# Kernel optimization log

Measured on AMD Instinct MI355X. Metric: run time of the kernel, lower is better.

The kernel has to match this reference:

```python
import jax, jax.numpy as jnp
import numpy as np


def setup_inputs() -> dict:
    key = jax.random.key(0)
    kA, kB = jax.random.split(key)
    B, H, W, C = 8, 48, 48, 256
    feature_A = jax.random.normal(kA, (B, H, W, C), dtype=jnp.float32)
    feature_B = jax.random.normal(kB, (B, H, W, C), dtype=jnp.float32)
    return {"feature_A": feature_A, "feature_B": feature_B}


def reference(feature_A, feature_B):
    # corr[b,i,j,k,l] = mean_c A[b,i,j,c] * B[b,k,l,c]
    # Expressed as a batched GEMM over the channel dim instead of the
    # naive [B,H,W,H,W,C] broadcast intermediate.
    C = feature_A.shape[-1]
    corr = jnp.einsum('bijc,bklc->bijkl', feature_A, feature_B) / C
    # L2 norm over source positions (i,j) per target position (k,l)
    penalty = jnp.sqrt(jnp.sum(corr * corr, axis=(1, 2), keepdims=True))  # [B,1,1,H,W]
    return corr / penalty
```

## Files before the change

kernel.cpp:

```cpp
#include <hip/hip_runtime.h>


#define HW2 2304
#define CH  256
#define NB  8
#define NELEM (NB * HW2 * CH)
#define KS  6

typedef __attribute__((ext_vector_type(8))) short bf16x8;
typedef __attribute__((ext_vector_type(4))) float f32x4;

static __device__ inline unsigned short f2bf(float f) {
    union { float f; unsigned u; } x; x.f = f;
    unsigned r = x.u + 0x7FFFu + ((x.u >> 16) & 1u);
    return (unsigned short)(r >> 16);
}

static __device__ inline float bf2f(unsigned short u) {
    union { unsigned u; float f; } x; x.u = ((unsigned)u) << 16;
    return x.f;
}

static __device__ inline void async_copy16(const void* g, void* l) {
    __builtin_amdgcn_global_load_lds(
        (const __attribute__((address_space(1))) unsigned int*)g,
        (__attribute__((address_space(3))) unsigned int*)l, 16, 0, 0);
}

__global__ __launch_bounds__(256) void convert_bf16(const float* __restrict__ A,
                                                    const float* __restrict__ B,
                                                    unsigned short* __restrict__ Abf,
                                                    unsigned short* __restrict__ Bbf,
                                                    unsigned short* __restrict__ Atbf) {
    __shared__ unsigned short t[64][65];
    const int blk = blockIdx.x;
    const bool isA = blk < 1152;
    const int tb = isA ? blk : blk - 1152;
    const int b  = tb / 144;
    const int tt = tb % 144;
    const int ijt = tt >> 2, ct = tt & 3;
    const size_t base = ((size_t)b * HW2 + (size_t)ijt * 64) * CH + ct * 64;
    const float* src = (isA ? A : B) + base;
    unsigned short* dst = (isA ? Abf : Bbf) + base;
    const int tid = threadIdx.x;
    const int lr = tid & 15, rq = tid >> 4;
#pragma unroll
    for (int p = 0; p < 4; p++) {
        const int row = rq + p * 16;
        float4 v = *(const float4*)(src + (size_t)row * CH + lr * 4);
        ushort4 u;
        u.x = f2bf(v.x); u.y = f2bf(v.y); u.z = f2bf(v.z); u.w = f2bf(v.w);
        *(ushort4*)(dst + (size_t)row * CH + lr * 4) = u;
        if (isA) {
            t[row][lr * 4 + 0] = u.x; t[row][lr * 4 + 1] = u.y;
            t[row][lr * 4 + 2] = u.z; t[row][lr * 4 + 3] = u.w;
        }
    }
    if (isA) {
        __syncthreads();
#pragma unroll
        for (int p = 0; p < 4; p++) {
            const int c = rq + p * 16;
            ushort4 u;
            u.x = t[lr * 4 + 0][c]; u.y = t[lr * 4 + 1][c];
            u.z = t[lr * 4 + 2][c]; u.w = t[lr * 4 + 3][c];
            *(ushort4*)(Atbf + ((size_t)b * CH + (size_t)(ct * 64 + c)) * HW2
                        + (size_t)ijt * 64 + lr * 4) = u;
        }
    }
}

__global__ __launch_bounds__(256) void gram_partial(const unsigned short* __restrict__ Atbf,
                                                    float* __restrict__ Gf) {
    __shared__ unsigned short As[2 * 128 * 32];
    __shared__ unsigned short Bs[2 * 128 * 32];
    const int tid = threadIdx.x;
    const int bx = blockIdx.x, by = blockIdx.y;
    const int b  = blockIdx.z / KS, ks = blockIdx.z % KS;
    const int kt0 = ks * (HW2 / KS);

    const unsigned short* Ar = Atbf + ((size_t)b * CH + by * 128) * HW2;
    const unsigned short* Br = Atbf + ((size_t)b * CH + bx * 128) * HW2;

    const int srow = tid >> 2, skcol = (tid & 3) * 8;
    const int wave = tid >> 6, lane = tid & 63;
    const int wm = (wave >> 1) * 64, wn = (wave & 1) * 64;
    const int lr = lane & 15, quad = lane >> 4, k8 = quad * 8;

    f32x4 acc[4][4];
#pragma unroll
    for (int i = 0; i < 4; i++)
#pragma unroll
        for (int j = 0; j < 4; j++) acc[i][j] = (f32x4){0.f, 0.f, 0.f, 0.f};

    for (int kt = kt0; kt < kt0 + HW2 / KS; kt += 64) {
#pragma unroll
        for (int c = 0; c < 2; c++) {
            const int kof = kt + c * 32;
#pragma unroll
            for (int i = 0; i < 2; i++) {
                async_copy16(Ar + (size_t)(srow + i * 64) * HW2 + kof + skcol,
                             &As[c * 4096 + tid * 8 + i * 2048]);
                async_copy16(Br + (size_t)(srow + i * 64) * HW2 + kof + skcol,
                             &Bs[c * 4096 + tid * 8 + i * 2048]);
            }
        }
        __syncthreads();
#pragma unroll
        for (int c = 0; c < 2; c++) {
            bf16x8 af[4], bfr[4];
#pragma unroll
            for (int mt = 0; mt < 4; mt++)
                af[mt] = *(const bf16x8*)&As[c * 4096 + (wm + mt * 16 + lr) * 32 + k8];
#pragma unroll
            for (int nt = 0; nt < 4; nt++)
                bfr[nt] = *(const bf16x8*)&Bs[c * 4096 + (wn + nt * 16 + lr) * 32 + k8];
#pragma unroll
            for (int mt = 0; mt < 4; mt++)
#pragma unroll
                for (int nt = 0; nt < 4; nt++)
                    acc[mt][nt] = __builtin_amdgcn_mfma_f32_16x16x32_bf16(
                        af[mt], bfr[nt], acc[mt][nt], 0, 0, 0);
        }
        __syncthreads();
    }
#pragma unroll
    for (int mt = 0; mt < 4; mt++)
#pragma unroll
        for (int nt = 0; nt < 4; nt++) {
            f32x4 v = acc[mt][nt];
            const int row = by * 128 + wm + mt * 16 + quad * 4;
            const int col = bx * 128 + wn + nt * 16 + lr;
#pragma unroll
            for (int r = 0; r < 4; r++)
                atomicAdd(&Gf[((size_t)b * CH + row + r) * CH + col], v[r]);
        }
}

__global__ __launch_bounds__(256) void g_to_bf(const float* __restrict__ Gf,
                                               unsigned short* __restrict__ Gbf) {
    const int i = blockIdx.x * 256 + threadIdx.x;
    float4 v = ((const float4*)Gf)[i];
    ushort4 u;
    u.x = f2bf(v.x); u.y = f2bf(v.y); u.z = f2bf(v.z); u.w = f2bf(v.w);
    ((ushort4*)Gbf)[i] = u;
}

__global__ __launch_bounds__(256) void colsq_pass(const unsigned short* __restrict__ Bbf,
                                                  const unsigned short* __restrict__ Gbf,
                                                  float* __restrict__ colSqG) {
    __shared__ unsigned short As[2 * 128 * 32];
    __shared__ unsigned short Bs[2 * 128 * 32];
    const int tid = threadIdx.x;
    const int bx = blockIdx.x;
    const int by = blockIdx.y;
    const int b  = blockIdx.z;

    const unsigned short* Ab = Bbf + ((size_t)b * HW2 + by * 128) * CH;
    const unsigned short* Gb = Gbf + ((size_t)b * CH + bx * 128) * CH;

    const int srow = tid >> 2, skcol = (tid & 3) * 8;
    const int wave = tid >> 6, lane = tid & 63;
    const int wm = (wave >> 1) * 64, wn = (wave & 1) * 64;
    const int lr = lane & 15, quad = lane >> 4, k8 = quad * 8;

    f32x4 acc[4][4];
#pragma unroll
    for (int i = 0; i < 4; i++)
#pragma unroll
        for (int j = 0; j < 4; j++) acc[i][j] = (f32x4){0.f, 0.f, 0.f, 0.f};

    for (int kt = 0; kt < CH; kt += 64) {
#pragma unroll
        for (int c = 0; c < 2; c++) {
            const int kof = kt + c * 32;
#pragma unroll
            for (int i = 0; i < 2; i++) {
                async_copy16(Ab + (size_t)(srow + i * 64) * CH + kof + skcol,
                             &As[c * 4096 + tid * 8 + i * 2048]);
                async_copy16(Gb + (size_t)(srow + i * 64) * CH + kof + skcol,
                             &Bs[c * 4096 + tid * 8 + i * 2048]);
            }
        }
        __syncthreads();
#pragma unroll
        for (int c = 0; c < 2; c++) {
            bf16x8 af[4], bfr[4];
#pragma unroll
            for (int mt = 0; mt < 4; mt++)
                af[mt] = *(const bf16x8*)&As[c * 4096 + (wm + mt * 16 + lr) * 32 + k8];
#pragma unroll
            for (int nt = 0; nt < 4; nt++)
                bfr[nt] = *(const bf16x8*)&Bs[c * 4096 + (wn + nt * 16 + lr) * 32 + k8];
#pragma unroll
            for (int mt = 0; mt < 4; mt++)
#pragma unroll
                for (int nt = 0; nt < 4; nt++)
                    acc[mt][nt] = __builtin_amdgcn_mfma_f32_16x16x32_bf16(
                        af[mt], bfr[nt], acc[mt][nt], 0, 0, 0);
        }
        __syncthreads();
    }

    const unsigned short* Brow = Ab + bx * 128;
#pragma unroll
    for (int mt = 0; mt < 4; mt++)
#pragma unroll
        for (int r = 0; r < 4; r++) {
            const int row = wm + mt * 16 + quad * 4 + r;
            float s = 0.f;
#pragma unroll
            for (int nt = 0; nt < 4; nt++) {
                const int col = wn + nt * 16 + lr;
                s += acc[mt][nt][r] * bf2f(Brow[(size_t)row * CH + col]);
            }
            s += __shfl_xor(s, 1); s += __shfl_xor(s, 2);
            s += __shfl_xor(s, 4); s += __shfl_xor(s, 8);
            if (lr == 0)
                atomicAdd(&colSqG[(size_t)b * HW2 + by * 128 + row], s);
        }
}

__global__ __launch_bounds__(256) void corr_out(const unsigned short* __restrict__ Abf,
                                                const unsigned short* __restrict__ Bbf,
                                                const float* __restrict__ colSqG,
                                                float* __restrict__ out) {
    __shared__ unsigned short As[2 * 128 * 32];
    __shared__ unsigned short Bs[2 * 128 * 32];
    const int tid = threadIdx.x;

    const int lin = blockIdx.x + 18 * (blockIdx.y + 18 * blockIdx.z);
    const int b  = lin & 7;
    const int r_ = lin >> 3;
    const int bx = r_ % 18;
    const int by = r_ / 18;

    const unsigned short* Ab = Abf + ((size_t)b * HW2 + (size_t)by * 128) * CH;
    const unsigned short* Bb = Bbf + ((size_t)b * HW2 + (size_t)bx * 128) * CH;

    const int srow = tid >> 2, skcol = (tid & 3) * 8;
    const int wave = tid >> 6, lane = tid & 63;
    const int wm = (wave >> 1) * 64, wn = (wave & 1) * 64;
    const int lr = lane & 15, quad = lane >> 4, k8 = quad * 8;

    f32x4 acc[4][4];
#pragma unroll
    for (int i = 0; i < 4; i++)
#pragma unroll
        for (int j = 0; j < 4; j++) acc[i][j] = (f32x4){0.f, 0.f, 0.f, 0.f};

    for (int kt = 0; kt < CH; kt += 64) {
#pragma unroll
        for (int c = 0; c < 2; c++) {
            const int kof = kt + c * 32;
#pragma unroll
            for (int i = 0; i < 2; i++) {
                async_copy16(Ab + (size_t)(srow + i * 64) * CH + kof + skcol,
                             &As[c * 4096 + tid * 8 + i * 2048]);
                async_copy16(Bb + (size_t)(srow + i * 64) * CH + kof + skcol,
                             &Bs[c * 4096 + tid * 8 + i * 2048]);
            }
        }
        __syncthreads();
#pragma unroll
        for (int c = 0; c < 2; c++) {
            bf16x8 af[4], bfr[4];
#pragma unroll
            for (int mt = 0; mt < 4; mt++)
                af[mt] = *(const bf16x8*)&As[c * 4096 + (wm + mt * 16 + lr) * 32 + k8];
#pragma unroll
            for (int nt = 0; nt < 4; nt++)
                bfr[nt] = *(const bf16x8*)&Bs[c * 4096 + (wn + nt * 16 + lr) * 32 + k8];
#pragma unroll
            for (int mt = 0; mt < 4; mt++)
#pragma unroll
                for (int nt = 0; nt < 4; nt++)
                    acc[mt][nt] = __builtin_amdgcn_mfma_f32_16x16x32_bf16(
                        af[mt], bfr[nt], acc[mt][nt], 0, 0, 0);
        }
        __syncthreads();
    }

    const int colBase = bx * 128 + wn;
    const size_t outBase = (size_t)b * HW2 * HW2;
#pragma unroll
    for (int nt = 0; nt < 4; nt++) {
        const int col = colBase + nt * 16 + lr;
        const float rinv = rsqrtf(colSqG[(size_t)b * HW2 + col]);
#pragma unroll
        for (int mt = 0; mt < 4; mt++) {
            const int row0 = by * 128 + wm + mt * 16 + quad * 4;
            f32x4 v = acc[mt][nt];
#pragma unroll
            for (int r = 0; r < 4; r++)
                out[outBase + (size_t)(row0 + r) * HW2 + col] = v[r] * rinv;
        }
    }
}

extern "C" void kernel_launch(void* const* d_in, const int* in_sizes, int n_in,
                              void* d_out, int out_size, void* d_ws, size_t ws_size,
                              hipStream_t stream) {
    const float* A = (const float*)d_in[0];
    const float* B = (const float*)d_in[1];
    float* out = (float*)d_out;

    unsigned short* Abf  = (unsigned short*)d_ws;
    unsigned short* Bbf  = Abf + NELEM;
    unsigned short* Atbf = Bbf + NELEM;
    unsigned short* Gbf  = Atbf + NELEM;
    float* Gf     = (float*)(Gbf + (size_t)NB * CH * CH);
    float* colSqG = Gf + (size_t)NB * CH * CH;

    hipMemsetAsync(Gf, 0, (size_t)NB * CH * CH * sizeof(float), stream);
    hipMemsetAsync(colSqG, 0, (size_t)NB * HW2 * sizeof(float), stream);

    convert_bf16<<<2304, 256, 0, stream>>>(A, B, Abf, Bbf, Atbf);
    gram_partial<<<dim3(2, 2, NB * KS), 256, 0, stream>>>(Atbf, Gf);
    g_to_bf<<<512, 256, 0, stream>>>(Gf, Gbf);
    colsq_pass<<<dim3(2, 18, NB), 256, 0, stream>>>(Bbf, Gbf, colSqG);
    corr_out<<<dim3(18, 18, NB), 256, 0, stream>>>(Abf, Bbf, colSqG, out);
}
```

Before: 254.5 us.

## Double-buffer GEMM stages, drop atomics and memsets, enlarge output tiles

The Gram kernel now computes full-K 64x64 tiles per block and writes bf16 directly. This removes the split-K float atomics, the zeroing memset and the separate conversion kernel. The colsq kernel uses 64-row tiles, reduces in shared memory and writes two partial column-norm arrays instead of using global atomics, which also removes the second memset. All three GEMMs get double-buffered async LDS loads so the next tile loads while the current one computes. corr_out moves to 128x256 tiles with launch_bounds(256,2), trading more accumulator registers and LDS for fewer B reloads. The Gram kernel now launches only 128 blocks with a long serial K loop, which may leave much of the GPU idle.

```diff
diff --git a/kernel.cpp b/kernel.cpp
--- a/kernel.cpp
+++ b/kernel.cpp
@@ -5,7 +5,6 @@
 #define CH  256
 #define NB  8
 #define NELEM (NB * HW2 * CH)
-#define KS  6
 
 typedef __attribute__((ext_vector_type(8))) short bf16x8;
 typedef __attribute__((ext_vector_type(4))) float f32x4;
@@ -70,130 +69,124 @@
     }
 }
 
-__global__ __launch_bounds__(256) void gram_partial(const unsigned short* __restrict__ Atbf,
-                                                    float* __restrict__ Gf) {
-    __shared__ unsigned short As[2 * 128 * 32];
-    __shared__ unsigned short Bs[2 * 128 * 32];
+__global__ __launch_bounds__(256) void gram(const unsigned short* __restrict__ Atbf,
+                                            unsigned short* __restrict__ Gbf) {
+    __shared__ unsigned short As[2][4096];
+    __shared__ unsigned short Bs[2][4096];
     const int tid = threadIdx.x;
-    const int bx = blockIdx.x, by = blockIdx.y;
-    const int b  = blockIdx.z / KS, ks = blockIdx.z % KS;
-    const int kt0 = ks * (HW2 / KS);
-
-    const unsigned short* Ar = Atbf + ((size_t)b * CH + by * 128) * HW2;
-    const unsigned short* Br = Atbf + ((size_t)b * CH + bx * 128) * HW2;
-
+    const int bx = blockIdx.x, by = blockIdx.y, b = blockIdx.z;
+    const unsigned short* Ar = Atbf + ((size_t)b * CH + by * 64) * HW2;
+    const unsigned short* Br = Atbf + ((size_t)b * CH + bx * 64) * HW2;
     const int srow = tid >> 2, skcol = (tid & 3) * 8;
     const int wave = tid >> 6, lane = tid & 63;
-    const int wm = (wave >> 1) * 64, wn = (wave & 1) * 64;
+    const int wm = (wave >> 1) * 32, wn = (wave & 1) * 32;
     const int lr = lane & 15, quad = lane >> 4, k8 = quad * 8;
 
-    f32x4 acc[4][4];
-#pragma unroll
-    for (int i = 0; i < 4; i++)
-#pragma unroll
-        for (int j = 0; j < 4; j++) acc[i][j] = (f32x4){0.f, 0.f, 0.f, 0.f};
-
-    for (int kt = kt0; kt < kt0 + HW2 / KS; kt += 64) {
-#pragma unroll
-        for (int c = 0; c < 2; c++) {
-            const int kof = kt + c * 32;
-#pragma unroll
-            for (int i = 0; i < 2; i++) {
-                async_copy16(Ar + (size_t)(srow + i * 64) * HW2 + kof + skcol,
-                             &As[c * 4096 + tid * 8 + i * 2048]);
-                async_copy16(Br + (size_t)(srow + i * 64) * HW2 + kof + skcol,
-                             &Bs[c * 4096 + tid * 8 + i * 2048]);
-            }
-        }
-        __syncthreads();
-#pragma unroll
-        for (int c = 0; c < 2; c++) {
-            bf16x8 af[4], bfr[4];
-#pragma unroll
-            for (int mt = 0; mt < 4; mt++)
-                af[mt] = *(const bf16x8*)&As[c * 4096 + (wm + mt * 16 + lr) * 32 + k8];
-#pragma unroll
-            for (int nt = 0; nt < 4; nt++)
-                bfr[nt] = *(const bf16x8*)&Bs[c * 4096 + (wn + nt * 16 + lr) * 32 + k8];
-#pragma unroll
-            for (int mt = 0; mt < 4; mt++)
-#pragma unroll
-                for (int nt = 0; nt < 4; nt++)
+    f32x4 acc[2][2];
+#pragma unroll
+    for (int i = 0; i < 2; i++)
+#pragma unroll
+        for (int j = 0; j < 2; j++) acc[i][j] = (f32x4){0.f, 0.f, 0.f, 0.f};
+
+#define G_STAGE(bufi, kt)                                                      \
+    {                                                                          \
+        _Pragma("unroll")                                                      \
+        for (int c2 = 0; c2 < 2; c2++) {                                       \
+            async_copy16(Ar + (size_t)srow * HW2 + (kt) + c2 * 32 + skcol,     \
+                         &As[bufi][c2 * 2048 + tid * 8]);                      \
+            async_copy16(Br + (size_t)srow * HW2 + (kt) + c2 * 32 + skcol,     \
+                         &Bs[bufi][c2 * 2048 + tid * 8]);                      \
+        }                                                                      \
+    }
+
+    G_STAGE(0, 0);
+    __syncthreads();
+    for (int t = 0; t < 36; t++) {
+        const int buf = t & 1;
+        if (t < 35) G_STAGE(buf ^ 1, (t + 1) * 64);
+#pragma unroll
+        for (int c2 = 0; c2 < 2; c2++) {
+            bf16x8 af[2], bfr[2];
+#pragma unroll
+            for (int mt = 0; mt < 2; mt++)
+                af[mt] = *(const bf16x8*)&As[buf][c2 * 2048 + (wm + mt * 16 + lr) * 32 + k8];
+#pragma unroll
+            for (int nt = 0; nt < 2; nt++)
+                bfr[nt] = *(const bf16x8*)&Bs[buf][c2 * 2048 + (wn + nt * 16 + lr) * 32 + k8];
+#pragma unroll
+            for (int mt = 0; mt < 2; mt++)
+#pragma unroll
+                for (int nt = 0; nt < 2; nt++)
                     acc[mt][nt] = __builtin_amdgcn_mfma_f32_16x16x32_bf16(
                         af[mt], bfr[nt], acc[mt][nt], 0, 0, 0);
         }
         __syncthreads();
     }
 #pragma unroll
-    for (int mt = 0; mt < 4; mt++)
-#pragma unroll
-        for (int nt = 0; nt < 4; nt++) {
-            f32x4 v = acc[mt][nt];
-            const int row = by * 128 + wm + mt * 16 + quad * 4;
-            const int col = bx * 128 + wn + nt * 16 + lr;
+    for (int mt = 0; mt < 2; mt++)
+#pragma unroll
+        for (int nt = 0; nt < 2; nt++) {
+            const int row = by * 64 + wm + mt * 16 + quad * 4;
+            const int col = bx * 64 + wn + nt * 16 + lr;
 #pragma unroll
             for (int r = 0; r < 4; r++)
-                atomicAdd(&Gf[((size_t)b * CH + row + r) * CH + col], v[r]);
-        }
-}
-
-__global__ __launch_bounds__(256) void g_to_bf(const float* __restrict__ Gf,
-                                               unsigned short* __restrict__ Gbf) {
-    const int i = blockIdx.x * 256 + threadIdx.x;
-    float4 v = ((const float4*)Gf)[i];
-    ushort4 u;
-    u.x = f2bf(v.x); u.y = f2bf(v.y); u.z = f2bf(v.z); u.w = f2bf(v.w);
-    ((ushort4*)Gbf)[i] = u;
-}
-
-__global__ __launch_bounds__(256) void colsq_pass(const unsigned short* __restrict__ Bbf,
-                                                  const unsigned short* __restrict__ Gbf,
-                                                  float* __restrict__ colSqG) {
-    __shared__ unsigned short As[2 * 128 * 32];
-    __shared__ unsigned short Bs[2 * 128 * 32];
+                Gbf[((size_t)b * CH + row + r) * CH + col] = f2bf(acc[mt][nt][r]);
+        }
+}
+
+__global__ __launch_bounds__(256) void colsq(const unsigned short* __restrict__ Bbf,
+                                             const unsigned short* __restrict__ Gbf,
+                                             float* __restrict__ cs0,
+                                             float* __restrict__ cs1) {
+    __shared__ unsigned short As[2][4096];
+    __shared__ unsigned short Bs[2][8192];
+    __shared__ float colSqL[64];
     const int tid = threadIdx.x;
     const int bx = blockIdx.x;
     const int by = blockIdx.y;
     const int b  = blockIdx.z;
-
-    const unsigned short* Ab = Bbf + ((size_t)b * HW2 + by * 128) * CH;
+    const unsigned short* Ab = Bbf + ((size_t)b * HW2 + by * 64) * CH;
     const unsigned short* Gb = Gbf + ((size_t)b * CH + bx * 128) * CH;
-
     const int srow = tid >> 2, skcol = (tid & 3) * 8;
     const int wave = tid >> 6, lane = tid & 63;
-    const int wm = (wave >> 1) * 64, wn = (wave & 1) * 64;
+    const int wm = (wave >> 1) * 32, wn = (wave & 1) * 64;
     const int lr = lane & 15, quad = lane >> 4, k8 = quad * 8;
 
-    f32x4 acc[4][4];
-#pragma unroll
-    for (int i = 0; i < 4; i++)
+    f32x4 acc[2][4];
+#pragma unroll
+    for (int i = 0; i < 2; i++)
 #pragma unroll
         for (int j = 0; j < 4; j++) acc[i][j] = (f32x4){0.f, 0.f, 0.f, 0.f};
 
-    for (int kt = 0; kt < CH; kt += 64) {
-#pragma unroll
-        for (int c = 0; c < 2; c++) {
-            const int kof = kt + c * 32;
-#pragma unroll
-            for (int i = 0; i < 2; i++) {
-                async_copy16(Ab + (size_t)(srow + i * 64) * CH + kof + skcol,
-                             &As[c * 4096 + tid * 8 + i * 2048]);
-                async_copy16(Gb + (size_t)(srow + i * 64) * CH + kof + skcol,
-                             &Bs[c * 4096 + tid * 8 + i * 2048]);
-            }
-        }
-        __syncthreads();
-#pragma unroll
-        for (int c = 0; c < 2; c++) {
-            bf16x8 af[4], bfr[4];
-#pragma unroll
-            for (int mt = 0; mt < 4; mt++)
-                af[mt] = *(const bf16x8*)&As[c * 4096 + (wm + mt * 16 + lr) * 32 + k8];
+#define C_STAGE(bufi, kt)                                                      \
+    {                                                                          \
+        _Pragma("unroll")                                                      \
+        for (int c2 = 0; c2 < 2; c2++) {                                       \
+            async_copy16(Ab + (size_t)srow * CH + (kt) + c2 * 32 + skcol,      \
+                         &As[bufi][c2 * 2048 + tid * 8]);                      \
+            _Pragma("unroll")                                                  \
+            for (int i = 0; i < 2; i++)                                        \
+                async_copy16(Gb + (size_t)(srow + i * 64) * CH + (kt) + c2 * 32 + skcol, \
+                             &Bs[bufi][c2 * 4096 + tid * 8 + i * 2048]);       \
+        }                                                                      \
+    }
+
+    C_STAGE(0, 0);
+    __syncthreads();
+    for (int t = 0; t < 4; t++) {
+        const int buf = t & 1;
+        if (t < 3) C_STAGE(buf ^ 1, (t + 1) * 64);
+#pragma unroll
+        for (int c2 = 0; c2 < 2; c2++) {
+            bf16x8 af[2], bfr[4];
+#pragma unroll
+            for (int mt = 0; mt < 2; mt++)
+                af[mt] = *(const bf16x8*)&As[buf][c2 * 2048 + (wm + mt * 16 + lr) * 32 + k8];
 #pragma unroll
             for (int nt = 0; nt < 4; nt++)
-                bfr[nt] = *(const bf16x8*)&Bs[c * 4096 + (wn + nt * 16 + lr) * 32 + k8];
-#pragma unroll
-            for (int mt = 0; mt < 4; mt++)
+                bfr[nt] = *(const bf16x8*)&Bs[buf][c2 * 4096 + (wn + nt * 16 + lr) * 32 + k8];
+#pragma unroll
+            for (int mt = 0; mt < 2; mt++)
 #pragma unroll
                 for (int nt = 0; nt < 4; nt++)
                     acc[mt][nt] = __builtin_amdgcn_mfma_f32_16x16x32_bf16(
@@ -202,91 +195,97 @@
         __syncthreads();
     }
 
-    const unsigned short* Brow = Ab + bx * 128;
-#pragma unroll
-    for (int mt = 0; mt < 4; mt++)
+    if (tid < 64) colSqL[tid] = 0.f;
+    __syncthreads();
+#pragma unroll
+    for (int mt = 0; mt < 2; mt++)
 #pragma unroll
         for (int r = 0; r < 4; r++) {
-            const int row = wm + mt * 16 + quad * 4 + r;
+            const int lrow = wm + mt * 16 + quad * 4 + r;
             float s = 0.f;
 #pragma unroll
             for (int nt = 0; nt < 4; nt++) {
-                const int col = wn + nt * 16 + lr;
-                s += acc[mt][nt][r] * bf2f(Brow[(size_t)row * CH + col]);
+                const int col = bx * 128 + wn + nt * 16 + lr;
+                s += acc[mt][nt][r] * bf2f(Ab[(size_t)lrow * CH + col]);
             }
             s += __shfl_xor(s, 1); s += __shfl_xor(s, 2);
             s += __shfl_xor(s, 4); s += __shfl_xor(s, 8);
-            if (lr == 0)
-                atomicAdd(&colSqG[(size_t)b * HW2 + by * 128 + row], s);
-        }
-}
-
-__global__ __launch_bounds__(256) void corr_out(const unsigned short* __restrict__ Abf,
-                                                const unsigned short* __restrict__ Bbf,
-                                                const float* __restrict__ colSqG,
-                                                float* __restrict__ out) {
-    __shared__ unsigned short As[2 * 128 * 32];
-    __shared__ unsigned short Bs[2 * 128 * 32];
+            if (lr == 0) atomicAdd(&colSqL[lrow], s);
+        }
+    __syncthreads();
+    if (tid < 64)
+        (bx == 0 ? cs0 : cs1)[(size_t)b * HW2 + by * 64 + tid] = colSqL[tid];
+}
+
+__global__ __launch_bounds__(256, 2) void corr_out(const unsigned short* __restrict__ Abf,
+                                                   const unsigned short* __restrict__ Bbf,
+                                                   const float* __restrict__ cs0,
+                                                   const float* __restrict__ cs1,
+                                                   float* __restrict__ out) {
+    __shared__ unsigned short As[2][4096];
+    __shared__ unsigned short Bs[2][8192];
     const int tid = threadIdx.x;
 
-    const int lin = blockIdx.x + 18 * (blockIdx.y + 18 * blockIdx.z);
+    const int lin = blockIdx.x + 9 * (blockIdx.y + 18 * blockIdx.z);
     const int b  = lin & 7;
     const int r_ = lin >> 3;
-    const int bx = r_ % 18;
-    const int by = r_ / 18;
+    const int bx = r_ % 9;
+    const int by = r_ / 9;
 
     const unsigned short* Ab = Abf + ((size_t)b * HW2 + (size_t)by * 128) * CH;
-    const unsigned short* Bb = Bbf + ((size_t)b * HW2 + (size_t)bx * 128) * CH;
+    const unsigned short* Bb = Bbf + ((size_t)b * HW2 + (size_t)bx * 256) * CH;
 
     const int srow = tid >> 2, skcol = (tid & 3) * 8;
     const int wave = tid >> 6, lane = tid & 63;
-    const int wm = (wave >> 1) * 64, wn = (wave & 1) * 64;
+    const int wm = (wave >> 1) * 64, wn = (wave & 1) * 128;
     const int lr = lane & 15, quad = lane >> 4, k8 = quad * 8;
 
-    f32x4 acc[4][4];
+    f32x4 acc[4][8];
 #pragma unroll
     for (int i = 0; i < 4; i++)
 #pragma unroll
-        for (int j = 0; j < 4; j++) acc[i][j] = (f32x4){0.f, 0.f, 0.f, 0.f};
-
-    for (int kt = 0; kt < CH; kt += 64) {
-#pragma unroll
-        for (int c = 0; c < 2; c++) {
-            const int kof = kt + c * 32;
-#pragma unroll
-            for (int i = 0; i < 2; i++) {
-                async_copy16(Ab + (size_t)(srow + i * 64) * CH + kof + skcol,
-                             &As[c * 4096 + tid * 8 + i * 2048]);
-                async_copy16(Bb + (size_t)(srow + i * 64) * CH + kof + skcol,
-                             &Bs[c * 4096 + tid * 8 + i * 2048]);
-            }
-        }
+        for (int j = 0; j < 8; j++) acc[i][j] = (f32x4){0.f, 0.f, 0.f, 0.f};
+
+#define O_STAGE(bufi, kt)                                                      \
+    {                                                                          \
+        _Pragma("unroll")                                                      \
+        for (int i = 0; i < 2; i++)                                            \
+            async_copy16(Ab + (size_t)(srow + i * 64) * CH + (kt) + skcol,     \
+                         &As[bufi][tid * 8 + i * 2048]);                       \
+        _Pragma("unroll")                                                      \
+        for (int i = 0; i < 4; i++)                                            \
+            async_copy16(Bb + (size_t)(srow + i * 64) * CH + (kt) + skcol,     \
+                         &Bs[bufi][tid * 8 + i * 2048]);                       \
+    }
+
+    O_STAGE(0, 0);
+    __syncthreads();
+    for (int t = 0; t < 8; t++) {
+        const int buf = t & 1;
+        if (t < 7) O_STAGE(buf ^ 1, (t + 1) * 32);
+        bf16x8 af[4], bfr[8];
+#pragma unroll
+        for (int mt = 0; mt < 4; mt++)
+            af[mt] = *(const bf16x8*)&As[buf][(wm + mt * 16 + lr) * 32 + k8];
+#pragma unroll
+        for (int nt = 0; nt < 8; nt++)
+            bfr[nt] = *(const bf16x8*)&Bs[buf][(wn + nt * 16 + lr) * 32 + k8];
+#pragma unroll
+        for (int mt = 0; mt < 4; mt++)
+#pragma unroll
+            for (int nt = 0; nt < 8; nt++)
+                acc[mt][nt] = __builtin_amdgcn_mfma_f32_16x16x32_bf16(
+                    af[mt], bfr[nt], acc[mt][nt], 0, 0, 0);
         __syncthreads();
-#pragma unroll
-        for (int c = 0; c < 2; c++) {
-            bf16x8 af[4], bfr[4];
-#pragma unroll
-            for (int mt = 0; mt < 4; mt++)
-                af[mt] = *(const bf16x8*)&As[c * 4096 + (wm + mt * 16 + lr) * 32 + k8];
-#pragma unroll
-            for (int nt = 0; nt < 4; nt++)
-                bfr[nt] = *(const bf16x8*)&Bs[c * 4096 + (wn + nt * 16 + lr) * 32 + k8];
-#pragma unroll
-            for (int mt = 0; mt < 4; mt++)
-#pragma unroll
-                for (int nt = 0; nt < 4; nt++)
-                    acc[mt][nt] = __builtin_amdgcn_mfma_f32_16x16x32_bf16(
-                        af[mt], bfr[nt], acc[mt][nt], 0, 0, 0);
-        }
-        __syncthreads();
-    }
-
-    const int colBase = bx * 128 + wn;
+    }
+
     const size_t outBase = (size_t)b * HW2 * HW2;
-#pragma unroll
-    for (int nt = 0; nt < 4; nt++) {
-        const int col = colBase + nt * 16 + lr;
-        const float rinv = rsqrtf(colSqG[(size_t)b * HW2 + col]);
+    const float* c0 = cs0 + (size_t)b * HW2;
+    const float* c1 = cs1 + (size_t)b * HW2;
+#pragma unroll
+    for (int nt = 0; nt < 8; nt++) {
+        const int col = bx * 256 + wn + nt * 16 + lr;
+        const float rinv = rsqrtf(c0[col] + c1[col]);
 #pragma unroll
         for (int mt = 0; mt < 4; mt++) {
             const int row0 = by * 128 + wm + mt * 16 + quad * 4;
@@ -309,15 +308,11 @@
     unsigned short* Bbf  = Abf + NELEM;
     unsigned short* Atbf = Bbf + NELEM;
     unsigned short* Gbf  = Atbf + NELEM;
-    float* Gf     = (float*)(Gbf + (size_t)NB * CH * CH);
-    float* colSqG = Gf + (size_t)NB * CH * CH;
-
-    hipMemsetAsync(Gf, 0, (size_t)NB * CH * CH * sizeof(float), stream);
-    hipMemsetAsync(colSqG, 0, (size_t)NB * HW2 * sizeof(float), stream);
+    float* cs0 = (float*)(Gbf + (size_t)NB * CH * CH);
+    float* cs1 = cs0 + (size_t)NB * HW2;
 
     convert_bf16<<<2304, 256, 0, stream>>>(A, B, Abf, Bbf, Atbf);
-    gram_partial<<<dim3(2, 2, NB * KS), 256, 0, stream>>>(Atbf, Gf);
-    g_to_bf<<<512, 256, 0, stream>>>(Gf, Gbf);
-    colsq_pass<<<dim3(2, 18, NB), 256, 0, stream>>>(Bbf, Gbf, colSqG);
-    corr_out<<<dim3(18, 18, NB), 256, 0, stream>>>(Abf, Bbf, colSqG, out);
-}
+    gram<<<dim3(4, 4, NB), 256, 0, stream>>>(Atbf, Gbf);
+    colsq<<<dim3(2, 36, NB), 256, 0, stream>>>(Bbf, Gbf, cs0, cs1);
+    corr_out<<<dim3(9, 18, NB), 256, 0, stream>>>(Abf, Bbf, cs0, cs1, out);
+}
```

Measured after the change: 254.6 us. Within noise of the previous version (+0.1%).
